# Kernel tuning notes

Measured on AMD Instinct MI355X. Metric: run time of the kernel, lower is better.

The kernel has to match this reference:

```python
import jax, jax.numpy as jnp
import numpy as np
from jax import lax

STRIDE = 1
PAD = 1


def setup_inputs() -> dict:
    key = jax.random.key(0)
    ks = jax.random.split(key, 6)
    B, C, H, W = 32, 256, 56, 56
    E, O, K = 4, 256, 3
    HID = max(C // 4, 8)  # 64
    return {
        "x": jax.random.normal(ks[0], (B, C, H, W), dtype=jnp.float32),
        "experts": jax.random.normal(ks[1], (E, O, C, K, K), dtype=jnp.float32),
        "rw1": jax.random.normal(ks[2], (HID, C), dtype=jnp.float32) * 0.05,
        "rb1": jax.random.normal(ks[3], (HID,), dtype=jnp.float32) * 0.05,
        "rw2": jax.random.normal(ks[4], (E, HID), dtype=jnp.float32) * 0.05,
        "rb2": jax.random.normal(ks[5], (E,), dtype=jnp.float32) * 0.05,
    }


def reference(x, experts, rw1, rb1, rw2, rb2):
    B, C, H, W = x.shape
    E, O, _, K, _ = experts.shape
    # Routing: global avg pool -> 1x1 conv (matmul) -> relu -> 1x1 conv -> softmax
    pooled = x.mean(axis=(2, 3))                      # [B, C]
    h = jax.nn.relu(pooled @ rw1.T + rb1)             # [B, HID]
    routing = jax.nn.softmax(h @ rw2.T + rb2, axis=-1)  # [B, E]
    # Per-sample mixed conv weights: [B, O, C, K, K]
    combined = jnp.einsum('be,eocij->bocij', routing, experts)
    # Per-sample conv as a single grouped conv: groups = B
    x_g = x.reshape(1, B * C, H, W)
    w_g = combined.reshape(B * O, C, K, K)
    out = lax.conv_general_dilated(
        x_g, w_g,
        window_strides=(STRIDE, STRIDE),
        padding=[(PAD, PAD), (PAD, PAD)],
        dimension_numbers=('NCHW', 'OIHW', 'NCHW'),
        feature_group_count=B,
    )  # [1, B*O, H', W']
    Ho, Wo = out.shape[2], out.shape[3]
    return out.reshape(B, O, Ho, Wo)
```

## Files before the change

### kernel.cpp

```cpp
#include <hip/hip_runtime.h>


#define B_  32
#define C_  256
#define H_  56
#define W_  56
#define HW_ 3136
#define E_  4
#define O_  256
#define HID_ 64
#define HP_ 58
#define PHW_ 3364
#define KK_ 2304

typedef __attribute__((ext_vector_type(8))) short bf16x8;
typedef __attribute__((ext_vector_type(4))) float f32x4;

__device__ __forceinline__ unsigned short f2bf(float f) {
    unsigned int u = __float_as_uint(f);
    u = (u + 0x7FFFu + ((u >> 16) & 1u)) >> 16;
    return (unsigned short)u;
}

__device__ __forceinline__ void load_lds16(const void* g, void* l) {
    __builtin_amdgcn_global_load_lds(
        (__attribute__((address_space(1))) unsigned int*)(unsigned long long)(const char*)g,
        (__attribute__((address_space(3))) unsigned int*)l,
        16, 0, 0);
}

__global__ void init_ws(unsigned short* __restrict__ xp, float* __restrict__ pooled) {
    const int b = blockIdx.x;
    const int t = threadIdx.x;
    pooled[b * C_ + t] = 0.0f;
    unsigned int* base = (unsigned int*)(xp + (size_t)b * PHW_ * C_);
    for (int i = t; i < HP_ * 128; i += 256) {
        base[i] = 0u;
        base[57 * HP_ * 128 + i] = 0u;
    }
    for (int i = t; i < 56 * 128; i += 256) {
        int hp = 1 + (i >> 7);
        int cc = i & 127;
        base[(hp * HP_ + 0) * 128 + cc]  = 0u;
        base[(hp * HP_ + 57) * 128 + cc] = 0u;
    }
}

__global__ void transform_pool(const float* __restrict__ x,
                               unsigned short* __restrict__ xp,
                               float* __restrict__ pooled) {
    const int h    = blockIdx.x;
    const int half = blockIdx.y;
    const int b    = blockIdx.z;
    const int t    = threadIdx.x;
    const int c0   = half * 128;
    __shared__ float tile[128 * 57];

    const float* src = x + ((size_t)(b * C_ + c0) * H_ + h) * W_;
#pragma unroll
    for (int i = t; i < 128 * 14; i += 256) {
        const int c  = i / 14;
        const int w4 = (i % 14) * 4;
        float4 v = *(const float4*)(src + (size_t)c * (H_ * W_) + w4);
        tile[c * 57 + w4 + 0] = v.x;
        tile[c * 57 + w4 + 1] = v.y;
        tile[c * 57 + w4 + 2] = v.z;
        tile[c * 57 + w4 + 3] = v.w;
    }
    __syncthreads();

    const int cu = t & 63;
    const int ws = t >> 6;
    float s0 = 0.f, s1 = 0.f;
    unsigned int* ob = (unsigned int*)xp
        + ((size_t)(b * HP_ + h + 1) * HP_ + 1) * (C_ / 2) + (c0 >> 1) + cu;
#pragma unroll
    for (int w = ws * 14; w < ws * 14 + 14; ++w) {
        float f0 = tile[(2 * cu + 0) * 57 + w];
        float f1 = tile[(2 * cu + 1) * 57 + w];
        s0 += f0; s1 += f1;
        ob[(size_t)w * (C_ / 2)] =
            (unsigned int)f2bf(f0) | ((unsigned int)f2bf(f1) << 16);
    }
    atomicAdd(&pooled[b * C_ + c0 + 2 * cu + 0], s0);
    atomicAdd(&pooled[b * C_ + c0 + 2 * cu + 1], s1);
}

__global__ void routing_kernel(const float* __restrict__ pooled,
                               const float* __restrict__ rw1,
                               const float* __restrict__ rb1,
                               const float* __restrict__ rw2,
                               const float* __restrict__ rb2,
                               float* __restrict__ routing) {
    const int b = blockIdx.x;
    const int t = threadIdx.x;
    __shared__ float pl[C_];
    __shared__ float part[256];
    __shared__ float hb[HID_];
    __shared__ float lg[E_];
    pl[t] = pooled[b * C_ + t] * (1.0f / (float)HW_);
    __syncthreads();
    const int j = t >> 2, seg = t & 3;
    {
        const float* w = rw1 + j * C_ + seg * 64;
        const float* p = pl + seg * 64;
        float s = 0.0f;
#pragma unroll 8
        for (int cc = 0; cc < 64; ++cc) s += p[cc] * w[cc];
        part[t] = s;
    }
    __syncthreads();
    if (seg == 0) {
        float s = part[t] + part[t + 1] + part[t + 2] + part[t + 3] + rb1[j];
        hb[j] = fmaxf(s, 0.0f);
    }
    __syncthreads();
    if (t < E_) {
        float s = rb2[t];
        for (int jj = 0; jj < HID_; ++jj) s += hb[jj] * rw2[t * HID_ + jj];
        lg[t] = s;
    }
    __syncthreads();
    if (t == 0) {
        float mx = fmaxf(fmaxf(lg[0], lg[1]), fmaxf(lg[2], lg[3]));
        float e0 = expf(lg[0] - mx), e1 = expf(lg[1] - mx);
        float e2 = expf(lg[2] - mx), e3 = expf(lg[3] - mx);
        float inv = 1.0f / (e0 + e1 + e2 + e3);
        routing[b * E_ + 0] = e0 * inv;
        routing[b * E_ + 1] = e1 * inv;
        routing[b * E_ + 2] = e2 * inv;
        routing[b * E_ + 3] = e3 * inv;
    }
}

__global__ void combine_kernel(const float* __restrict__ experts,
                               const float* __restrict__ routing,
                               unsigned short* __restrict__ wcomb) {
    const int o = blockIdx.x;
    const int c = threadIdx.x;
    __shared__ float rt[B_ * E_];
    if (c < B_ * E_) rt[c] = routing[c];
    __syncthreads();

    float w[E_][9];
#pragma unroll
    for (int e = 0; e < E_; ++e) {
        const float* ep = experts + ((size_t)(e * O_ + o) * C_ + c) * 9;
        float4 v0 = *(const float4*)(ep + 0);
        float4 v1 = *(const float4*)(ep + 4);
        w[e][0] = v0.x; w[e][1] = v0.y; w[e][2] = v0.z; w[e][3] = v0.w;
        w[e][4] = v1.x; w[e][5] = v1.y; w[e][6] = v1.z; w[e][7] = v1.w;
        w[e][8] = ep[8];
    }
    for (int b = 0; b < B_; ++b) {
        const float r0 = rt[b * 4 + 0], r1 = rt[b * 4 + 1];
        const float r2 = rt[b * 4 + 2], r3 = rt[b * 4 + 3];
        unsigned short* wp = wcomb + (size_t)(b * O_ + o) * KK_ + c;
#pragma unroll
        for (int k = 0; k < 9; ++k) {
            float a = r0 * w[0][k] + r1 * w[1][k] + r2 * w[2][k] + r3 * w[3][k];
            wp[(size_t)k * C_] = f2bf(a);
        }
    }
}

__global__ __launch_bounds__(256) void conv_gemm(const unsigned short* __restrict__ xp,
                                                 const unsigned short* __restrict__ wcomb,
                                                 float* __restrict__ out) {
    __shared__ alignas(16) unsigned short Alds[128 * 64];
    __shared__ alignas(16) unsigned short Blds[128 * 64];

    const int tid  = threadIdx.x;
    const int lane = tid & 63;
    const int wid  = tid >> 6;

    const int id = blockIdx.x;
    const int b  = (id >> 3) / 50 * 8 + (id & 7);
    const int t  = (id >> 3) % 50;
    const int o0 = (t & 1) * 128;
    const int n0 = (t >> 1) * 128;

    const int qg = (lane & 7) ^ ((lane >> 3) & 7);

    const unsigned short* aptr = wcomb
        + (size_t)(b * O_ + o0 + wid * 32 + (lane >> 3)) * KK_ + qg * 8;
    const unsigned short* bptr = xp + (size_t)b * PHW_ * C_ + qg * 8;
    unsigned int boff[4];
#pragma unroll
    for (int iss = 0; iss < 4; ++iss) {
        int p = n0 + wid * 32 + iss * 8 + (lane >> 3);
        if (p > HW_ - 1) p = HW_ - 1;
        boff[iss] = (unsigned int)((p / W_) * HP_ + (p % W_)) * C_;
    }
    unsigned short* aldst = (unsigned short*)Alds + (wid * 32) * 64;
    unsigned short* bldst = (unsigned short*)Blds + (wid * 32) * 64;

    f32x4 acc[4][4];
#pragma unroll
    for (int i = 0; i < 4; ++i)
#pragma unroll
        for (int j = 0; j < 4; ++j) acc[i][j] = (f32x4){0.f, 0.f, 0.f, 0.f};

    const int fm = lane & 15;
    const int fq = lane >> 4;
    const int wm = wid >> 1, wn = wid & 1;
    const int colk0 = ((0 + fq) ^ (fm & 7)) * 8;
    const int colk1 = ((4 + fq) ^ (fm & 7)) * 8;
    const unsigned short* ardb = (const unsigned short*)Alds + (wm * 64 + fm) * 64;
    const unsigned short* brdb = (const unsigned short*)Blds + (wn * 64 + fm) * 64;

    for (int kc = 0; kc < 36; ++kc) {
        const int r   = kc >> 2;
        const int duA = kc * 64;
        const int duB = ((r / 3) * HP_ + (r % 3)) * C_ + (kc & 3) * 64;
        __syncthreads();
#pragma unroll
        for (int iss = 0; iss < 4; ++iss) {
            load_lds16(aptr + (size_t)iss * (8 * KK_) + duA, aldst + iss * (8 * 64));
            load_lds16(bptr + boff[iss] + duB,              bldst + iss * (8 * 64));
        }
        __syncthreads();
#pragma unroll
        for (int ks = 0; ks < 2; ++ks) {
            const int col = ks ? colk1 : colk0;
            bf16x8 af[4], bv[4];
#pragma unroll
            for (int mi = 0; mi < 4; ++mi) af[mi] = *(const bf16x8*)(ardb + mi * (16 * 64) + col);
#pragma unroll
            for (int ni = 0; ni < 4; ++ni) bv[ni] = *(const bf16x8*)(brdb + ni * (16 * 64) + col);
#pragma unroll
            for (int mi = 0; mi < 4; ++mi)
#pragma unroll
                for (int ni = 0; ni < 4; ++ni)
                    acc[mi][ni] = __builtin_amdgcn_mfma_f32_16x16x32_bf16(
                        af[mi], bv[ni], acc[mi][ni], 0, 0, 0);
        }
    }

#pragma unroll
    for (int ni = 0; ni < 4; ++ni) {
        const int n = n0 + wn * 64 + ni * 16 + fm;
        if (n >= HW_) continue;
#pragma unroll
        for (int mi = 0; mi < 4; ++mi) {
            const int m = o0 + wm * 64 + mi * 16 + fq * 4;
            float* po = out + (size_t)(b * O_ + m) * HW_ + n;
#pragma unroll
            for (int rg = 0; rg < 4; ++rg) po[(size_t)rg * HW_] = acc[mi][ni][rg];
        }
    }
}

extern "C" void kernel_launch(void* const* d_in, const int* in_sizes, int n_in,
                              void* d_out, int out_size, void* d_ws, size_t ws_size,
                              hipStream_t stream) {
    const float* x       = (const float*)d_in[0];
    const float* experts = (const float*)d_in[1];
    const float* rw1     = (const float*)d_in[2];
    const float* rb1     = (const float*)d_in[3];
    const float* rw2     = (const float*)d_in[4];
    const float* rb2     = (const float*)d_in[5];
    float* out = (float*)d_out;

    const size_t XP_OFF = 0;
    const size_t WC_OFF = 55115776;
    const size_t PL_OFF = WC_OFF + 37748736;
    const size_t RT_OFF = PL_OFF + 32768;
    unsigned short* xp    = (unsigned short*)((char*)d_ws + XP_OFF);
    unsigned short* wcomb = (unsigned short*)((char*)d_ws + WC_OFF);
    float* pooled  = (float*)((char*)d_ws + PL_OFF);
    float* routing = (float*)((char*)d_ws + RT_OFF);

    init_ws<<<dim3(B_), dim3(256), 0, stream>>>(xp, pooled);
    transform_pool<<<dim3(H_, 2, B_), dim3(256), 0, stream>>>(x, xp, pooled);
    routing_kernel<<<dim3(B_), dim3(256), 0, stream>>>(pooled, rw1, rb1, rw2, rb2, routing);
    combine_kernel<<<dim3(O_), dim3(256), 0, stream>>>(experts, routing, wcomb);
    conv_gemm<<<dim3(1600), dim3(256), 0, stream>>>(xp, wcomb, out);
}
```

Baseline: 378.5 us.

## Fold padding init into transform, drop atomics, parallelize combine, bound conv occupancy

Removes the separate init_ws kernel by zeroing the padded border of xp inside transform_pool. Pooling atomics are replaced with per-row partial sums in a workspace buffer, which routing_kernel then reduces. combine_kernel now spreads the batch dimension across a second grid axis and stages each sample's weights in LDS so they can be written with 16-byte stores. conv_gemm gains a launch-bounds occupancy hint of 4 blocks, which could force register pressure or spilling.

Result: faster. 323.3 us (-14.6%).

```diff
diff --git a/kernel.cpp b/kernel.cpp
--- a/kernel.cpp
+++ b/kernel.cpp
@@ -29,32 +29,16 @@
         16, 0, 0);
 }
 
-__global__ void init_ws(unsigned short* __restrict__ xp, float* __restrict__ pooled) {
-    const int b = blockIdx.x;
-    const int t = threadIdx.x;
-    pooled[b * C_ + t] = 0.0f;
-    unsigned int* base = (unsigned int*)(xp + (size_t)b * PHW_ * C_);
-    for (int i = t; i < HP_ * 128; i += 256) {
-        base[i] = 0u;
-        base[57 * HP_ * 128 + i] = 0u;
-    }
-    for (int i = t; i < 56 * 128; i += 256) {
-        int hp = 1 + (i >> 7);
-        int cc = i & 127;
-        base[(hp * HP_ + 0) * 128 + cc]  = 0u;
-        base[(hp * HP_ + 57) * 128 + cc] = 0u;
-    }
-}
-
 __global__ void transform_pool(const float* __restrict__ x,
                                unsigned short* __restrict__ xp,
-                               float* __restrict__ pooled) {
+                               float* __restrict__ pp) {
     const int h    = blockIdx.x;
     const int half = blockIdx.y;
     const int b    = blockIdx.z;
     const int t    = threadIdx.x;
     const int c0   = half * 128;
     __shared__ float tile[128 * 57];
+    __shared__ float part[4][128];
 
     const float* src = x + ((size_t)(b * C_ + c0) * H_ + h) * W_;
 #pragma unroll
@@ -67,6 +51,23 @@
         tile[c * 57 + w4 + 2] = v.z;
         tile[c * 57 + w4 + 3] = v.w;
     }
+
+    unsigned int* ubase = (unsigned int*)(xp + (size_t)b * PHW_ * C_);
+    {
+        const int hp = h + 1;
+        if (t < 128) {
+            const int col = (t >> 6) ? 57 : 0;
+            const int cu  = t & 63;
+            ubase[((size_t)hp * HP_ + col) * 128 + half * 64 + cu] = 0u;
+        }
+        if (h == 0) {
+            for (int i = t; i < HP_ * 64; i += 256) {
+                const int pix = i >> 6, cu = i & 63;
+                ubase[(size_t)pix * 128 + half * 64 + cu] = 0u;
+                ubase[((size_t)57 * HP_ + pix) * 128 + half * 64 + cu] = 0u;
+            }
+        }
+    }
     __syncthreads();
 
     const int cu = t & 63;
@@ -82,11 +83,16 @@
         ob[(size_t)w * (C_ / 2)] =
             (unsigned int)f2bf(f0) | ((unsigned int)f2bf(f1) << 16);
     }
-    atomicAdd(&pooled[b * C_ + c0 + 2 * cu + 0], s0);
-    atomicAdd(&pooled[b * C_ + c0 + 2 * cu + 1], s1);
-}
-
-__global__ void routing_kernel(const float* __restrict__ pooled,
+    part[ws][2 * cu + 0] = s0;
+    part[ws][2 * cu + 1] = s1;
+    __syncthreads();
+    if (t < 128) {
+        float v = part[0][t] + part[1][t] + part[2][t] + part[3][t];
+        pp[((size_t)(b * C_ + c0 + t)) * 56 + h] = v;
+    }
+}
+
+__global__ void routing_kernel(const float* __restrict__ pp,
                                const float* __restrict__ rw1,
                                const float* __restrict__ rb1,
                                const float* __restrict__ rw2,
@@ -98,7 +104,16 @@
     __shared__ float part[256];
     __shared__ float hb[HID_];
     __shared__ float lg[E_];
-    pl[t] = pooled[b * C_ + t] * (1.0f / (float)HW_);
+    {
+        const float* p = pp + (size_t)(b * C_ + t) * 56;
+        float s = 0.f;
+#pragma unroll
+        for (int i = 0; i < 14; ++i) {
+            float4 v = *(const float4*)(p + 4 * i);
+            s += v.x + v.y + v.z + v.w;
+        }
+        pl[t] = s * (1.0f / (float)HW_);
+    }
     __syncthreads();
     const int j = t >> 2, seg = t & 3;
     {
@@ -136,11 +151,12 @@
 __global__ void combine_kernel(const float* __restrict__ experts,
                                const float* __restrict__ routing,
                                unsigned short* __restrict__ wcomb) {
-    const int o = blockIdx.x;
-    const int c = threadIdx.x;
-    __shared__ float rt[B_ * E_];
-    if (c < B_ * E_) rt[c] = routing[c];
-    __syncthreads();
+    const int o  = blockIdx.x;
+    const int bg = blockIdx.y;
+    const int c  = threadIdx.x;
+    __shared__ alignas(16) unsigned short sh[KK_];
+    __shared__ float rt[16];
+    if (c < 16) rt[c] = routing[bg * 16 + c];
 
     float w[E_][9];
 #pragma unroll
@@ -152,21 +168,28 @@
         w[e][4] = v1.x; w[e][5] = v1.y; w[e][6] = v1.z; w[e][7] = v1.w;
         w[e][8] = ep[8];
     }
-    for (int b = 0; b < B_; ++b) {
-        const float r0 = rt[b * 4 + 0], r1 = rt[b * 4 + 1];
-        const float r2 = rt[b * 4 + 2], r3 = rt[b * 4 + 3];
-        unsigned short* wp = wcomb + (size_t)(b * O_ + o) * KK_ + c;
+    __syncthreads();
+#pragma unroll
+    for (int bq = 0; bq < 4; ++bq) {
+        const float r0 = rt[bq * 4 + 0], r1 = rt[bq * 4 + 1];
+        const float r2 = rt[bq * 4 + 2], r3 = rt[bq * 4 + 3];
 #pragma unroll
         for (int k = 0; k < 9; ++k) {
             float a = r0 * w[0][k] + r1 * w[1][k] + r2 * w[2][k] + r3 * w[3][k];
-            wp[(size_t)k * C_] = f2bf(a);
-        }
-    }
-}
-
-__global__ __launch_bounds__(256) void conv_gemm(const unsigned short* __restrict__ xp,
-                                                 const unsigned short* __restrict__ wcomb,
-                                                 float* __restrict__ out) {
+            sh[k * C_ + c] = f2bf(a);
+        }
+        __syncthreads();
+        const int b = bg * 4 + bq;
+        uint4* dst = (uint4*)(wcomb + (size_t)(b * O_ + o) * KK_);
+        const uint4* s4 = (const uint4*)sh;
+        for (int idx = c; idx < KK_ / 8; idx += 256) dst[idx] = s4[idx];
+        __syncthreads();
+    }
+}
+
+__global__ __launch_bounds__(256, 4) void conv_gemm(const unsigned short* __restrict__ xp,
+                                                    const unsigned short* __restrict__ wcomb,
+                                                    float* __restrict__ out) {
     __shared__ alignas(16) unsigned short Alds[128 * 64];
     __shared__ alignas(16) unsigned short Blds[128 * 64];
 
@@ -264,16 +287,15 @@
 
     const size_t XP_OFF = 0;
     const size_t WC_OFF = 55115776;
-    const size_t PL_OFF = WC_OFF + 37748736;
-    const size_t RT_OFF = PL_OFF + 32768;
+    const size_t PP_OFF = WC_OFF + 37748736;
+    const size_t RT_OFF = PP_OFF + 1835008;
     unsigned short* xp    = (unsigned short*)((char*)d_ws + XP_OFF);
     unsigned short* wcomb = (unsigned short*)((char*)d_ws + WC_OFF);
-    float* pooled  = (float*)((char*)d_ws + PL_OFF);
+    float* pp      = (float*)((char*)d_ws + PP_OFF);
     float* routing = (float*)((char*)d_ws + RT_OFF);
 
-    init_ws<<<dim3(B_), dim3(256), 0, stream>>>(xp, pooled);
-    transform_pool<<<dim3(H_, 2, B_), dim3(256), 0, stream>>>(x, xp, pooled);
-    routing_kernel<<<dim3(B_), dim3(256), 0, stream>>>(pooled, rw1, rb1, rw2, rb2, routing);
-    combine_kernel<<<dim3(O_), dim3(256), 0, stream>>>(experts, routing, wcomb);
+    transform_pool<<<dim3(H_, 2, B_), dim3(256), 0, stream>>>(x, xp, pp);
+    routing_kernel<<<dim3(B_), dim3(256), 0, stream>>>(pp, rw1, rb1, rw2, rb2, routing);
+    combine_kernel<<<dim3(O_, 8), dim3(256), 0, stream>>>(experts, routing, wcomb);
     conv_gemm<<<dim3(1600), dim3(256), 0, stream>>>(xp, wcomb, out);
 }
```
